# Kernel optimization log

Measured on AMD Instinct MI355X. Metric: run time of the kernel, lower is better.

Reference implementation:

```python
import jax, jax.numpy as jnp
import numpy as np

B, T, D = 4, 4096, 2048
NE = 64
TOP_K = 8


def setup_inputs() -> dict:
    key = jax.random.key(0)
    k1, k2 = jax.random.split(key)
    x = jax.random.normal(k1, (B, T, D), dtype=jnp.float32)
    w = jax.random.normal(k2, (NE, D), dtype=jnp.float32) * (1.0 / np.sqrt(D))
    gate_b = jnp.zeros((NE,), dtype=jnp.float32)
    return {"x": x, "w": w, "gate_b": gate_b, "top_k": TOP_K}


def reference(x, w, gate_b, top_k):
    # router logits: [b, t, ne]
    logits = jnp.einsum('nd,btd->btn', w, x)
    scores = jax.nn.sigmoid(logits) + gate_b
    weights, indices = jax.lax.top_k(scores, top_k)
    weights = weights / weights.sum(-1, keepdims=True)
    return (weights, indices, scores)
```

## Files before the change

kernel.cpp:

```cpp
#include <hip/hip_runtime.h>
#include <math.h>

#define D_DIM 2048
#define NE    64
#define NTOK  16384
#define TK    8
#define TOKB  64
#define HALF  1024
#define KCH   64
#define NCH   (HALF / KCH)
#define GT    1024

#define OUT_I_OFF (NTOK * TK)
#define OUT_S_OFF (2 * NTOK * TK)

#define GLOBAL_AS __attribute__((address_space(1)))
#define LDS_AS    __attribute__((address_space(3)))

static __device__ __forceinline__ void async_copy16(const float* g, float* l) {
    __builtin_amdgcn_global_load_lds((const GLOBAL_AS void*)g, (LDS_AS void*)l, 16, 0, 0);
}

__global__ __launch_bounds__(256) void wtrans_kernel(const float* __restrict__ w,
                                                     float* __restrict__ wt) {
    int i = blockIdx.x * 256 + threadIdx.x;
    int e  = i >> 9;
    int db = i & 511;
    float4 v = ((const float4*)w)[(size_t)e * 512 + db];
    int d = db * 4;
    wt[(size_t)(d + 0) * NE + e] = v.x;
    wt[(size_t)(d + 1) * NE + e] = v.y;
    wt[(size_t)(d + 2) * NE + e] = v.z;
    wt[(size_t)(d + 3) * NE + e] = v.w;
}

template <bool USE_WT>
__global__ __launch_bounds__(GT) void gate_gemm(const float* __restrict__ x,
                                                const float* __restrict__ w,
                                                const float* __restrict__ wt,
                                                const float* __restrict__ gb,
                                                float* __restrict__ scores) {
    __shared__ float xs[2][2][TOKB * KCH];

    const int tid  = threadIdx.x;
    const int lane = tid & 63;
    const int wv   = __builtin_amdgcn_readfirstlane(tid >> 6);
    const int g    = wv & 7;
    const int h    = wv >> 3;
    const int e0   = g * 8;
    const int tok0 = blockIdx.x * TOKB;
    const int l7   = lane & 7;

    const int st = tid >> 4;
    const int sq = tid & 15;
    const int dq = sq ^ (st & 7);
    const float* gx = x + (size_t)(tok0 + st) * D_DIM + (dq << 2);

    auto stage = [&](int c, int buf) {
        async_copy16(gx + 0 * HALF + c * KCH, &xs[buf][0][tid * 4]);
        async_copy16(gx + 1 * HALF + c * KCH, &xs[buf][1][tid * 4]);
    };

    auto loadw = [&](float* dst, int hd) {
        if (USE_WT) {
            const float* p = wt + (size_t)(h * HALF + hd) * NE + e0;
#pragma unroll
            for (int j = 0; j < 4; ++j)
#pragma unroll
                for (int e = 0; e < 8; ++e) dst[j * 8 + e] = p[j * NE + e];
        } else {
#pragma unroll
            for (int e = 0; e < 8; ++e) {
                const float* p = w + (size_t)(e0 + e) * D_DIM + h * HALF + hd;
#pragma unroll
                for (int j = 0; j < 4; ++j) dst[j * 8 + e] = p[j];
            }
        }
    };

    float acc[8];
#pragma unroll
    for (int e = 0; e < 8; ++e) acc[e] = 0.f;

    float wA[32], wB[32];
    loadw(wA, 0);
    stage(0, 0);

    for (int c = 0; c < NCH; ++c) {
        __syncthreads();
        if (c + 1 < NCH) stage(c + 1, (c + 1) & 1);
        const float* xrow = &xs[c & 1][h][lane * KCH];

        for (int dd = 0; dd < KCH; dd += 8) {
            const int hd = c * KCH + dd;
            loadw(wB, (hd + 4) & (HALF - 1));
            {
                float4 xq = *(const float4*)(xrow + ((((dd >> 2) + 0) ^ l7) << 2));
#pragma unroll
                for (int e = 0; e < 8; ++e) acc[e] = fmaf(xq.x, wA[0 * 8 + e], acc[e]);
#pragma unroll
                for (int e = 0; e < 8; ++e) acc[e] = fmaf(xq.y, wA[1 * 8 + e], acc[e]);
#pragma unroll
                for (int e = 0; e < 8; ++e) acc[e] = fmaf(xq.z, wA[2 * 8 + e], acc[e]);
#pragma unroll
                for (int e = 0; e < 8; ++e) acc[e] = fmaf(xq.w, wA[3 * 8 + e], acc[e]);
            }
            loadw(wA, (hd + 8) & (HALF - 1));
            {
                float4 xq = *(const float4*)(xrow + ((((dd >> 2) + 1) ^ l7) << 2));
#pragma unroll
                for (int e = 0; e < 8; ++e) acc[e] = fmaf(xq.x, wB[0 * 8 + e], acc[e]);
#pragma unroll
                for (int e = 0; e < 8; ++e) acc[e] = fmaf(xq.y, wB[1 * 8 + e], acc[e]);
#pragma unroll
                for (int e = 0; e < 8; ++e) acc[e] = fmaf(xq.z, wB[2 * 8 + e], acc[e]);
#pragma unroll
                for (int e = 0; e < 8; ++e) acc[e] = fmaf(xq.w, wB[3 * 8 + e], acc[e]);
            }
        }
    }

    __syncthreads();
    float* red = &xs[0][0][0];
    if (h == 1) {
#pragma unroll
        for (int e = 0; e < 8; ++e) red[g * 512 + lane * 8 + e] = acc[e];
    }
    __syncthreads();
    if (h == 0) {
        float sc[8];
#pragma unroll
        for (int e = 0; e < 8; ++e) {
            float v = acc[e] + red[g * 512 + lane * 8 + e];
            sc[e] = 1.f / (1.f + expf(-v)) + gb[e0 + e];
        }
        float* so = scores + (size_t)(tok0 + lane) * NE + e0;
        float4 v0 = {sc[0], sc[1], sc[2], sc[3]};
        float4 v1 = {sc[4], sc[5], sc[6], sc[7]};
        ((float4*)so)[0] = v0;
        ((float4*)so)[1] = v1;
    }
}

__global__ __launch_bounds__(256) void topk_kernel(const float* __restrict__ scores,
                                                   float* __restrict__ out) {
    const int tid = threadIdx.x;
    const int t   = blockIdx.x * 64 + (tid >> 2);
    const int q   = tid & 3;
    float v[16];
    const float4* sp = (const float4*)(scores + (size_t)t * NE + q * 16);
    float4 a = sp[0], b = sp[1], c = sp[2], d = sp[3];
    v[0] = a.x;  v[1] = a.y;  v[2] = a.z;  v[3] = a.w;
    v[4] = b.x;  v[5] = b.y;  v[6] = b.z;  v[7] = b.w;
    v[8] = c.x;  v[9] = c.y;  v[10] = c.z; v[11] = c.w;
    v[12] = d.x; v[13] = d.y; v[14] = d.z; v[15] = d.w;

    float kv[TK]; int ki[TK];
#pragma unroll
    for (int k = 0; k < TK; ++k) {
        float bv = v[0]; int bi = q * 16;
#pragma unroll
        for (int j = 1; j < 16; ++j) {
            bool gt = v[j] > bv;
            bv = gt ? v[j] : bv;
            bi = gt ? (q * 16 + j) : bi;
        }
#pragma unroll
        for (int off = 1; off < 4; off <<= 1) {
            float ov = __shfl_xor(bv, off);
            int   oi = __shfl_xor(bi, off);
            bool take = (ov > bv) || (ov == bv && oi < bi);
            bv = take ? ov : bv;
            bi = take ? oi : bi;
        }
        int lj = bi - q * 16;
#pragma unroll
        for (int j = 0; j < 16; ++j) v[j] = (j == lj) ? -3e38f : v[j];
        kv[k] = bv; ki[k] = bi;
    }

    if (q == 0) {
        float s = 0.f;
#pragma unroll
        for (int k = 0; k < TK; ++k) s += kv[k];
        float inv = 1.f / s;
        float* ow = out + (size_t)t * TK;
        float* oi = out + OUT_I_OFF + (size_t)t * TK;
#pragma unroll
        for (int k = 0; k < TK; ++k) {
            ow[k] = kv[k] * inv;
            oi[k] = (float)ki[k];
        }
    }
}

extern "C" void kernel_launch(void* const* d_in, const int* in_sizes, int n_in,
                              void* d_out, int out_size, void* d_ws, size_t ws_size,
                              hipStream_t stream) {
    const float* x  = (const float*)d_in[0];
    const float* w  = (const float*)d_in[1];
    const float* gb = (const float*)d_in[2];
    float* out    = (float*)d_out;
    float* scores = out + OUT_S_OFF;
    float* wtbuf  = (float*)d_ws;
    (void)in_sizes; (void)n_in; (void)out_size;

    const bool use_wt = ws_size >= (size_t)NE * D_DIM * sizeof(float);
    if (use_wt) {
        wtrans_kernel<<<dim3(128), dim3(256), 0, stream>>>(w, wtbuf);
        gate_gemm<true><<<dim3(NTOK / TOKB), dim3(GT), 0, stream>>>(x, w, wtbuf, gb, scores);
    } else {
        gate_gemm<false><<<dim3(NTOK / TOKB), dim3(GT), 0, stream>>>(x, w, wtbuf, gb, scores);
    }
    topk_kernel<<<dim3(NTOK / 64), dim3(256), 0, stream>>>(scores, out);
}
```

Measured before the change: 280.3 us.

## Restructure gate GEMM into 8-way split-K with 8x8 register tiles per thread

The gate GEMM moves to 512-thread blocks in which each wave owns one of eight K slices. Each thread computes an 8-token by 8-expert register tile, with weights read directly from the original row-major layout as float4s, so the separate weight transpose kernel and its launch are dropped. Partial sums from the eight K slices are reduced through padded LDS before the sigmoid. This raises arithmetic reuse per load, at the cost of more registers per thread, an 8-way LDS reduction and a smaller K chunk per barrier.

```diff
diff --git a/kernel.cpp b/kernel.cpp
--- a/kernel.cpp
+++ b/kernel.cpp
@@ -6,10 +6,15 @@
 #define NTOK  16384
 #define TK    8
 #define TOKB  64
-#define HALF  1024
-#define KCH   64
-#define NCH   (HALF / KCH)
-#define GT    1024
+#define KS    8
+#define KD    (D_DIM / KS)
+#define KCH   16
+#define NCH   (KD / KCH)
+#define BT    512
+
+#define XS_BUF_FLOATS (KS * TOKB * KCH)
+#define RED_ROW       72
+#define POOL_FLOATS   (KS * TOKB * RED_ROW)
 
 #define OUT_I_OFF (NTOK * TK)
 #define OUT_S_OFF (2 * NTOK * TK)
@@ -21,122 +26,124 @@
     __builtin_amdgcn_global_load_lds((const GLOBAL_AS void*)g, (LDS_AS void*)l, 16, 0, 0);
 }
 
-__global__ __launch_bounds__(256) void wtrans_kernel(const float* __restrict__ w,
-                                                     float* __restrict__ wt) {
-    int i = blockIdx.x * 256 + threadIdx.x;
-    int e  = i >> 9;
-    int db = i & 511;
-    float4 v = ((const float4*)w)[(size_t)e * 512 + db];
-    int d = db * 4;
-    wt[(size_t)(d + 0) * NE + e] = v.x;
-    wt[(size_t)(d + 1) * NE + e] = v.y;
-    wt[(size_t)(d + 2) * NE + e] = v.z;
-    wt[(size_t)(d + 3) * NE + e] = v.w;
-}
-
-template <bool USE_WT>
-__global__ __launch_bounds__(GT) void gate_gemm(const float* __restrict__ x,
-                                                const float* __restrict__ w,
-                                                const float* __restrict__ wt,
-                                                const float* __restrict__ gb,
-                                                float* __restrict__ scores) {
-    __shared__ float xs[2][2][TOKB * KCH];
+__global__ __launch_bounds__(BT, 2) void gate_gemm(const float* __restrict__ x,
+                                                   const float* __restrict__ w,
+                                                   const float* __restrict__ gb,
+                                                   float* __restrict__ scores) {
+    __shared__ __align__(16) float pool[POOL_FLOATS];
 
     const int tid  = threadIdx.x;
     const int lane = tid & 63;
-    const int wv   = __builtin_amdgcn_readfirstlane(tid >> 6);
-    const int g    = wv & 7;
-    const int h    = wv >> 3;
-    const int e0   = g * 8;
+    const int ks   = tid >> 6;
+    const int lt   = lane >> 3;
+    const int le   = lane & 7;
     const int tok0 = blockIdx.x * TOKB;
-    const int l7   = lane & 7;
-
-    const int st = tid >> 4;
-    const int sq = tid & 15;
-    const int dq = sq ^ (st & 7);
-    const float* gx = x + (size_t)(tok0 + st) * D_DIM + (dq << 2);
+    const int lt3  = lt & 3;
+
+    const float4* wp[8];
+#pragma unroll
+    for (int j = 0; j < 8; ++j)
+        wp[j] = (const float4*)(w + (size_t)(j * 8 + le) * D_DIM + ks * KD);
+
+    const float* srcb[4];
+#pragma unroll
+    for (int k = 0; k < 4; ++k) {
+        int qq  = tid + k * BT;
+        int kss = qq >> 8;
+        int r   = qq & 255;
+        int ts  = r >> 2;
+        int s   = r & 3;
+        int dqs = s ^ (ts & 3);
+        srcb[k] = x + (size_t)(tok0 + ts) * D_DIM + kss * KD + dqs * 4;
+    }
 
     auto stage = [&](int c, int buf) {
-        async_copy16(gx + 0 * HALF + c * KCH, &xs[buf][0][tid * 4]);
-        async_copy16(gx + 1 * HALF + c * KCH, &xs[buf][1][tid * 4]);
+        float* dst = pool + buf * XS_BUF_FLOATS + tid * 4;
+#pragma unroll
+        for (int k = 0; k < 4; ++k)
+            async_copy16(srcb[k] + c * KCH, dst + k * (BT * 4));
     };
 
-    auto loadw = [&](float* dst, int hd) {
-        if (USE_WT) {
-            const float* p = wt + (size_t)(h * HALF + hd) * NE + e0;
-#pragma unroll
-            for (int j = 0; j < 4; ++j)
-#pragma unroll
-                for (int e = 0; e < 8; ++e) dst[j * 8 + e] = p[j * NE + e];
-        } else {
-#pragma unroll
-            for (int e = 0; e < 8; ++e) {
-                const float* p = w + (size_t)(e0 + e) * D_DIM + h * HALF + hd;
-#pragma unroll
-                for (int j = 0; j < 4; ++j) dst[j * 8 + e] = p[j];
+    float acc[8][8];
+#pragma unroll
+    for (int i = 0; i < 8; ++i)
+#pragma unroll
+        for (int j = 0; j < 8; ++j) acc[i][j] = 0.f;
+
+    float4 wa[8], wb[8];
+#pragma unroll
+    for (int j = 0; j < 8; ++j) wa[j] = wp[j][0];
+    stage(0, 0);
+
+    auto step = [&](float4 (&WC)[8], float4 (&WN)[8], int c, int dq) {
+        const int c4n = (c * 4 + dq + 1) & 63;
+#pragma unroll
+        for (int j = 0; j < 8; ++j) WN[j] = wp[j][c4n];
+        const float* xb = pool + (c & 1) * XS_BUF_FLOATS + ks * (TOKB * KCH)
+                        + lt * KCH + ((dq ^ lt3) << 2);
+        float4 xi[8];
+#pragma unroll
+        for (int i = 0; i < 8; ++i)
+            xi[i] = *(const float4*)(xb + i * (8 * KCH));
+#pragma unroll
+        for (int i = 0; i < 8; ++i) {
+#pragma unroll
+            for (int j = 0; j < 8; ++j) {
+                acc[i][j] = fmaf(xi[i].x, WC[j].x, acc[i][j]);
+                acc[i][j] = fmaf(xi[i].y, WC[j].y, acc[i][j]);
+                acc[i][j] = fmaf(xi[i].z, WC[j].z, acc[i][j]);
+                acc[i][j] = fmaf(xi[i].w, WC[j].w, acc[i][j]);
             }
         }
     };
-
-    float acc[8];
-#pragma unroll
-    for (int e = 0; e < 8; ++e) acc[e] = 0.f;
-
-    float wA[32], wB[32];
-    loadw(wA, 0);
-    stage(0, 0);
 
     for (int c = 0; c < NCH; ++c) {
         __syncthreads();
         if (c + 1 < NCH) stage(c + 1, (c + 1) & 1);
-        const float* xrow = &xs[c & 1][h][lane * KCH];
-
-        for (int dd = 0; dd < KCH; dd += 8) {
-            const int hd = c * KCH + dd;
-            loadw(wB, (hd + 4) & (HALF - 1));
-            {
-                float4 xq = *(const float4*)(xrow + ((((dd >> 2) + 0) ^ l7) << 2));
-#pragma unroll
-                for (int e = 0; e < 8; ++e) acc[e] = fmaf(xq.x, wA[0 * 8 + e], acc[e]);
-#pragma unroll
-                for (int e = 0; e < 8; ++e) acc[e] = fmaf(xq.y, wA[1 * 8 + e], acc[e]);
-#pragma unroll
-                for (int e = 0; e < 8; ++e) acc[e] = fmaf(xq.z, wA[2 * 8 + e], acc[e]);
-#pragma unroll
-                for (int e = 0; e < 8; ++e) acc[e] = fmaf(xq.w, wA[3 * 8 + e], acc[e]);
-            }
-            loadw(wA, (hd + 8) & (HALF - 1));
-            {
-                float4 xq = *(const float4*)(xrow + ((((dd >> 2) + 1) ^ l7) << 2));
-#pragma unroll
-                for (int e = 0; e < 8; ++e) acc[e] = fmaf(xq.x, wB[0 * 8 + e], acc[e]);
-#pragma unroll
-                for (int e = 0; e < 8; ++e) acc[e] = fmaf(xq.y, wB[1 * 8 + e], acc[e]);
-#pragma unroll
-                for (int e = 0; e < 8; ++e) acc[e] = fmaf(xq.z, wB[2 * 8 + e], acc[e]);
-#pragma unroll
-                for (int e = 0; e < 8; ++e) acc[e] = fmaf(xq.w, wB[3 * 8 + e], acc[e]);
-            }
-        }
+        step(wa, wb, c, 0);
+        step(wb, wa, c, 1);
+        step(wa, wb, c, 2);
+        step(wb, wa, c, 3);
     }
 
     __syncthreads();
-    float* red = &xs[0][0][0];
-    if (h == 1) {
-#pragma unroll
-        for (int e = 0; e < 8; ++e) red[g * 512 + lane * 8 + e] = acc[e];
+    {
+        const int rb = ks * (TOKB * RED_ROW);
+#pragma unroll
+        for (int i = 0; i < 8; ++i)
+#pragma unroll
+            for (int j = 0; j < 8; ++j)
+                pool[rb + (i * 8 + lt) * RED_ROW + j * 8 + le] = acc[i][j];
     }
     __syncthreads();
-    if (h == 0) {
-        float sc[8];
-#pragma unroll
-        for (int e = 0; e < 8; ++e) {
-            float v = acc[e] + red[g * 512 + lane * 8 + e];
-            sc[e] = 1.f / (1.f + expf(-v)) + gb[e0 + e];
-        }
-        float* so = scores + (size_t)(tok0 + lane) * NE + e0;
-        float4 v0 = {sc[0], sc[1], sc[2], sc[3]};
-        float4 v1 = {sc[4], sc[5], sc[6], sc[7]};
+    {
+        const int t = tid >> 3;
+        const int q = tid & 7;
+        float s[8];
+#pragma unroll
+        for (int u = 0; u < 8; ++u) s[u] = 0.f;
+#pragma unroll
+        for (int k = 0; k < KS; ++k) {
+            const float* rp = pool + k * (TOKB * RED_ROW) + t * RED_ROW + q * 8;
+            float4 a = *(const float4*)rp;
+            float4 b = *(const float4*)(rp + 4);
+            s[0] += a.x; s[1] += a.y; s[2] += a.z; s[3] += a.w;
+            s[4] += b.x; s[5] += b.y; s[6] += b.z; s[7] += b.w;
+        }
+        float4 g0 = *(const float4*)(gb + q * 8);
+        float4 g1 = *(const float4*)(gb + q * 8 + 4);
+        float r[8];
+        r[0] = 1.f / (1.f + expf(-s[0])) + g0.x;
+        r[1] = 1.f / (1.f + expf(-s[1])) + g0.y;
+        r[2] = 1.f / (1.f + expf(-s[2])) + g0.z;
+        r[3] = 1.f / (1.f + expf(-s[3])) + g0.w;
+        r[4] = 1.f / (1.f + expf(-s[4])) + g1.x;
+        r[5] = 1.f / (1.f + expf(-s[5])) + g1.y;
+        r[6] = 1.f / (1.f + expf(-s[6])) + g1.z;
+        r[7] = 1.f / (1.f + expf(-s[7])) + g1.w;
+        float* so = scores + (size_t)(tok0 + t) * NE + q * 8;
+        float4 v0 = {r[0], r[1], r[2], r[3]};
+        float4 v1 = {r[4], r[5], r[6], r[7]};
         ((float4*)so)[0] = v0;
         ((float4*)so)[1] = v1;
     }
@@ -202,15 +209,8 @@
     const float* gb = (const float*)d_in[2];
     float* out    = (float*)d_out;
     float* scores = out + OUT_S_OFF;
-    float* wtbuf  = (float*)d_ws;
-    (void)in_sizes; (void)n_in; (void)out_size;
-
-    const bool use_wt = ws_size >= (size_t)NE * D_DIM * sizeof(float);
-    if (use_wt) {
-        wtrans_kernel<<<dim3(128), dim3(256), 0, stream>>>(w, wtbuf);
-        gate_gemm<true><<<dim3(NTOK / TOKB), dim3(GT), 0, stream>>>(x, w, wtbuf, gb, scores);
-    } else {
-        gate_gemm<false><<<dim3(NTOK / TOKB), dim3(GT), 0, stream>>>(x, w, wtbuf, gb, scores);
-    }
+    (void)in_sizes; (void)n_in; (void)out_size; (void)d_ws; (void)ws_size;
+
+    gate_gemm<<<dim3(NTOK / TOKB), dim3(BT), 0, stream>>>(x, w, gb, scores);
     topk_kernel<<<dim3(NTOK / 64), dim3(256), 0, stream>>>(scores, out);
 }
```

Measured after the change: 320.6 us. 14.4% more time.
